# Performance work log

Measured on AMD Instinct MI355X. Metric: run time of the kernel, lower is better.

The kernel has to match this reference:

```python
import jax, jax.numpy as jnp
import numpy as np

N_NODES = 100000
N_EDGES = 250000
IN_CH = 256
OUT_CH = 256
REL_DIM = 1536
N_REL = 64
HIDDEN = IN_CH * 2  # 512
EPS = 1e-5


def setup_inputs() -> dict:
    key = jax.random.key(0)
    ks = jax.random.split(key, 12)
    s = 0.02
    return {
        "x": jax.random.normal(ks[0], (N_NODES, IN_CH), jnp.float32),
        "edge_index": jax.random.randint(ks[1], (2, N_EDGES), 0, N_NODES, jnp.int64),
        "edge_type": jax.random.randint(ks[2], (N_EDGES,), 0, N_REL, jnp.int64),
        "relation_embs": jax.random.normal(ks[3], (N_REL, REL_DIM), jnp.float32),
        "W1": jax.random.normal(ks[4], (IN_CH + REL_DIM, HIDDEN), jnp.float32) * s,
        "b1": jnp.zeros((HIDDEN,), jnp.float32),
        "W2": jax.random.normal(ks[5], (HIDDEN, OUT_CH), jnp.float32) * s,
        "b2": jnp.zeros((OUT_CH,), jnp.float32),
        "Ws": jax.random.normal(ks[6], (IN_CH, OUT_CH), jnp.float32) * s,
        "bs": jnp.zeros((OUT_CH,), jnp.float32),
        "gamma": jnp.ones((OUT_CH,), jnp.float32),
        "beta": jnp.zeros((OUT_CH,), jnp.float32),
    }


def reference(x, edge_index, edge_type, relation_embs, W1, b1, W2, b2, Ws, bs, gamma, beta):
    src, dst = edge_index[0], edge_index[1]
    # gather: per-edge inputs [E, in+rel]
    msg_in = jnp.concatenate([x[src], relation_embs[edge_type]], axis=-1)
    # message MLP: Linear -> ReLU -> Linear
    h = jax.nn.relu(msg_in @ W1 + b1)
    messages = h @ W2 + b2  # [E, out]
    # scatter_add into destination nodes
    agg = jax.ops.segment_sum(messages, dst, num_segments=x.shape[0])
    out = x @ Ws + bs + agg
    # LayerNorm (eps=1e-5) then ReLU
    mu = jnp.mean(out, axis=-1, keepdims=True)
    var = jnp.mean(jnp.square(out - mu), axis=-1, keepdims=True)
    out = (out - mu) * jax.lax.rsqrt(var + EPS) * gamma + beta
    return jax.nn.relu(out)
```

## Files before the change

kernel.cpp:

```cpp
#include <hip/hip_runtime.h>
#include <hip/hip_bf16.h>

#define IN_CHN 256
#define OUT_CHN 256
#define REL_DIM 1536
#define HIDN 512

using short8 = __attribute__((ext_vector_type(8))) short;
using f32x4  = __attribute__((ext_vector_type(4))) float;

__device__ __forceinline__ float bf2f(short s) {
    union { unsigned u; float f; } v;
    v.u = ((unsigned)(unsigned short)s) << 16;
    return v.f;
}
__device__ __forceinline__ unsigned cvt_pk_bf16(float a, float b) {
    unsigned r;
    asm("v_cvt_pk_bf16_f32 %0, %1, %2" : "=v"(r) : "v"(a), "v"(b));
    return r;
}
__device__ __forceinline__ unsigned short f2bf_s(float f) {
    union { float f; unsigned u; } v; v.f = f;
    unsigned u = v.u + 0x7FFFu + ((v.u >> 16) & 1u);
    return (unsigned short)(u >> 16);
}

__global__ void k_prep_w(const float* __restrict__ W1, const float* __restrict__ Ws,
                         const float* __restrict__ W2,
                         unsigned short* __restrict__ Bt, unsigned short* __restrict__ W2t,
                         unsigned short* __restrict__ Wst)
{
    int idx = blockIdx.x * 256 + threadIdx.x;
    const int n1 = HIDN * IN_CHN;
    const int n2 = OUT_CHN * HIDN;
    const int n3 = OUT_CHN * IN_CHN;
    if (idx < n1) {
        int j = idx >> 8, k = idx & 255;
        Bt[idx] = f2bf_s(W1[(size_t)k * HIDN + j]);
    } else if (idx < n1 + n2) {
        int t = idx - n1;
        int j = t >> 9, k = t & 511;
        W2t[t] = f2bf_s(W2[(size_t)k * OUT_CHN + j]);
    } else if (idx < n1 + n2 + n3) {
        int t = idx - n1 - n2;
        int j = t >> 8, k = t & 255;
        Wst[t] = f2bf_s(Ws[(size_t)k * OUT_CHN + j]);
    }
}

__global__ __launch_bounds__(512) void k_rel(const float* __restrict__ rel,
                                             const float* __restrict__ W1,
                                             const float* __restrict__ b1,
                                             unsigned short* __restrict__ Rb)
{
    __shared__ float s[REL_DIM];
    const int r = blockIdx.x;
    for (int i = threadIdx.x; i < REL_DIM; i += 512)
        s[i] = rel[(size_t)r * REL_DIM + i];
    __syncthreads();
    const int j = threadIdx.x;
    float acc = b1[j];
    const float* wp = W1 + (size_t)IN_CHN * HIDN + j;
#pragma unroll 8
    for (int k = 0; k < REL_DIM; ++k)
        acc = fmaf(s[k], wp[(size_t)k * HIDN], acc);
    Rb[r * HIDN + j] = f2bf_s(acc);
}

__global__ __launch_bounds__(512) void k_node(const float* __restrict__ x,
                                              const unsigned short* __restrict__ Bt,
                                              unsigned short* __restrict__ X1, int N)
{
    const int row0 = blockIdx.x * 64;
    const int tid = threadIdx.x;
    const int w = tid >> 6, l = tid & 63;
    const int l15 = l & 15, lg = l >> 4;
    const int colw = w * 64;

    const float* ap[4];
#pragma unroll
    for (int rf = 0; rf < 4; ++rf) {
        int row = row0 + 16 * rf + l15;
        if (row >= N) row = N - 1;
        ap[rf] = x + (size_t)row * IN_CHN + 8 * lg;
    }
    const unsigned short* bp[4];
#pragma unroll
    for (int cf = 0; cf < 4; ++cf)
        bp[cf] = Bt + (size_t)(colw + 16 * cf + l15) * IN_CHN + 8 * lg;

    f32x4 acc[4][4] = {};
    for (int k0 = 0; k0 < IN_CHN; k0 += 32) {
        short8 a[4], b[4];
#pragma unroll
        for (int rf = 0; rf < 4; ++rf) {
            float4 lo = *(const float4*)(ap[rf] + k0);
            float4 hi = *(const float4*)(ap[rf] + k0 + 4);
            union { short8 s; unsigned u[4]; } pk;
            pk.u[0] = cvt_pk_bf16(lo.x, lo.y);
            pk.u[1] = cvt_pk_bf16(lo.z, lo.w);
            pk.u[2] = cvt_pk_bf16(hi.x, hi.y);
            pk.u[3] = cvt_pk_bf16(hi.z, hi.w);
            a[rf] = pk.s;
        }
#pragma unroll
        for (int cf = 0; cf < 4; ++cf)
            b[cf] = *(const short8*)(bp[cf] + k0);
#pragma unroll
        for (int rf = 0; rf < 4; ++rf)
#pragma unroll
            for (int cf = 0; cf < 4; ++cf)
                acc[rf][cf] = __builtin_amdgcn_mfma_f32_16x16x32_bf16(a[rf], b[cf], acc[rf][cf], 0, 0, 0);
    }
#pragma unroll
    for (int rf = 0; rf < 4; ++rf) {
#pragma unroll
        for (int cf = 0; cf < 4; ++cf) {
            int col = colw + 16 * cf + l15;
#pragma unroll
            for (int r = 0; r < 4; ++r) {
                int row = row0 + 16 * rf + 4 * lg + r;
                if (row >= N) continue;
                X1[(size_t)row * HIDN + col] = f2bf_s(acc[rf][cf][r]);
            }
        }
    }
}

__global__ void k_hist(const int* __restrict__ ei, int* __restrict__ cnt, int E)
{
    int e = blockIdx.x * 256 + threadIdx.x;
    if (e < E) atomicAdd(&cnt[ei[E + e]], 1);
}

__global__ __launch_bounds__(512) void k_scan1(const int* __restrict__ cnt, int* __restrict__ offs,
                                               int* __restrict__ bsum, int N)
{
    __shared__ int s[512];
    int t = threadIdx.x;
    int i = blockIdx.x * 512 + t;
    int v = (i < N) ? cnt[i] : 0;
    s[t] = v;
    __syncthreads();
    for (int d = 1; d < 512; d <<= 1) {
        int a = (t >= d) ? s[t - d] : 0;
        __syncthreads();
        s[t] += a;
        __syncthreads();
    }
    if (i < N) offs[i] = s[t] - v;
    if (t == 511) bsum[blockIdx.x] = s[511];
}

__global__ __launch_bounds__(512) void k_scan2(int* __restrict__ bsum, int NB)
{
    __shared__ int s[512];
    int t = threadIdx.x;
    if (t < NB) s[t] = bsum[t];
    __syncthreads();
    if (t == 0) {
        int run = 0;
        for (int j = 0; j < NB; ++j) { int v = s[j]; s[j] = run; run += v; }
    }
    __syncthreads();
    if (t < NB) bsum[t] = s[t];
}

__global__ void k_scan3(int* __restrict__ offs, const int* __restrict__ bsum,
                        int* __restrict__ cursor, int N, int E)
{
    int i = blockIdx.x * 256 + threadIdx.x;
    if (i < N) {
        int v = offs[i] + bsum[i >> 9];
        offs[i] = v;
        cursor[i] = v;
    }
    if (i == 0) offs[N] = E;
}

__global__ void k_scatter(const int* __restrict__ ei, const int* __restrict__ et,
                          int* __restrict__ cursor, int* __restrict__ eperm, int E)
{
    int e = blockIdx.x * 256 + threadIdx.x;
    if (e < E) {
        int d = ei[E + e];
        int pos = atomicAdd(&cursor[d], 1);
        eperm[pos] = ei[e] | (et[e] << 20);
    }
}

__global__ __launch_bounds__(256, 6) void k_gather(const int* __restrict__ offs,
                                                   const int* __restrict__ eperm,
                                                   const unsigned short* __restrict__ X1,
                                                   const unsigned short* __restrict__ Rb,
                                                   unsigned short* __restrict__ Hagg, int N)
{
    const int g = (blockIdx.x * 256 + threadIdx.x) >> 6;
    const int l = threadIdx.x & 63;
    if (g >= N) return;
    const int o0 = offs[g], o1 = offs[g + 1];
    const int deg = o1 - o0;
    float a8[8] = {};
    for (int base = 0; base < deg; base += 64) {
        const int nk = min(64, deg - base);
        int pv = eperm[o0 + base + (l < nk ? l : nk - 1)];
        for (int e = 0; e < nk; e += 4) {
            int pvk[4];
#pragma unroll
            for (int k2 = 0; k2 < 4; ++k2)
                pvk[k2] = __shfl(pv, e + k2);
            short8 xa[4], ra[4];
#pragma unroll
            for (int k2 = 0; k2 < 4; ++k2) {
                if (e + k2 < nk) {
                    xa[k2] = *(const short8*)(X1 + (size_t)(pvk[k2] & 0xFFFFF) * HIDN + l * 8);
                    ra[k2] = *(const short8*)(Rb + (pvk[k2] >> 20) * HIDN + l * 8);
                }
            }
#pragma unroll
            for (int k2 = 0; k2 < 4; ++k2) {
                if (e + k2 < nk) {
#pragma unroll
                    for (int j = 0; j < 8; ++j)
                        a8[j] += fmaxf(bf2f(xa[k2][j]) + bf2f(ra[k2][j]), 0.f);
                }
            }
        }
    }
    union { short8 s; unsigned u[4]; } pk;
    pk.u[0] = cvt_pk_bf16(a8[0], a8[1]);
    pk.u[1] = cvt_pk_bf16(a8[2], a8[3]);
    pk.u[2] = cvt_pk_bf16(a8[4], a8[5]);
    pk.u[3] = cvt_pk_bf16(a8[6], a8[7]);
    *(short8*)(Hagg + (size_t)g * HIDN + l * 8) = pk.s;
}

__global__ __launch_bounds__(256) void k_out(const unsigned short* __restrict__ Hagg,
                                             const unsigned short* __restrict__ W2t,
                                             const unsigned short* __restrict__ Wst,
                                             const float* __restrict__ x,
                                             const int* __restrict__ offs,
                                             const float* __restrict__ b2,
                                             const float* __restrict__ bs,
                                             const float* __restrict__ gamma,
                                             const float* __restrict__ beta,
                                             float* __restrict__ out, int N)
{
    __shared__ unsigned short Alds[64][72];
    __shared__ float sdeg[64];
    __shared__ float sred[4][64], sqred[4][64];
    const int row0 = blockIdx.x * 64;
    const int tid = threadIdx.x;
    const int w = tid >> 6, l = tid & 63;
    const int l15 = l & 15, lg = l >> 4;
    const int colw = w * 64;

    if (tid < 64) {
        int g = row0 + tid;
        if (g >= N) g = N - 1;
        sdeg[tid] = (float)(offs[g + 1] - offs[g]);
    }

    const int srow = tid >> 2;
    int srowg = row0 + srow; if (srowg >= N) srowg = N - 1;
    const int sc = (tid & 3) * 16;
    const unsigned short* hsrc = Hagg + (size_t)srowg * HIDN + sc;
    const float* xsrc = x + (size_t)srowg * IN_CHN + sc;
    unsigned short* sdst0 = &Alds[srow][sc];
    unsigned short* sdst1 = &Alds[srow][sc + 8];

    const unsigned short* bp[4];
    const unsigned short* sp[4];
#pragma unroll
    for (int cf = 0; cf < 4; ++cf) {
        bp[cf] = W2t + (size_t)(colw + 16 * cf + l15) * HIDN + 8 * lg;
        sp[cf] = Wst + (size_t)(colw + 16 * cf + l15) * IN_CHN + 8 * lg;
    }
    const unsigned short* ard[4];
#pragma unroll
    for (int rf = 0; rf < 4; ++rf)
        ard[rf] = &Alds[16 * rf + l15][lg * 8];

    f32x4 acc[4][4] = {};
    short8 st0, st1;

    st0 = *(const short8*)(hsrc + 0);
    st1 = *(const short8*)(hsrc + 8);
    *(short8*)sdst0 = st0;
    *(short8*)sdst1 = st1;
    __syncthreads();
    for (int t = 0; t < 8; ++t) {
        if (t + 1 < 8) {
            st0 = *(const short8*)(hsrc + (t + 1) * 64);
            st1 = *(const short8*)(hsrc + (t + 1) * 64 + 8);
        }
#pragma unroll
        for (int kk = 0; kk < 2; ++kk) {
            short8 a[4], b[4];
#pragma unroll
            for (int rf = 0; rf < 4; ++rf)
                a[rf] = *(const short8*)(ard[rf] + kk * 32);
#pragma unroll
            for (int cf = 0; cf < 4; ++cf)
                b[cf] = *(const short8*)(bp[cf] + t * 64 + kk * 32);
#pragma unroll
            for (int rf = 0; rf < 4; ++rf)
#pragma unroll
                for (int cf = 0; cf < 4; ++cf)
                    acc[rf][cf] = __builtin_amdgcn_mfma_f32_16x16x32_bf16(a[rf], b[cf], acc[rf][cf], 0, 0, 0);
        }
        __syncthreads();
        if (t + 1 < 8) {
            *(short8*)sdst0 = st0;
            *(short8*)sdst1 = st1;
            __syncthreads();
        }
    }

    {
        float4 f0 = *(const float4*)(xsrc + 0);
        float4 f1 = *(const float4*)(xsrc + 4);
        float4 f2 = *(const float4*)(xsrc + 8);
        float4 f3 = *(const float4*)(xsrc + 12);
        union { short8 s; unsigned u[4]; } p0, p1;
        p0.u[0] = cvt_pk_bf16(f0.x, f0.y); p0.u[1] = cvt_pk_bf16(f0.z, f0.w);
        p0.u[2] = cvt_pk_bf16(f1.x, f1.y); p0.u[3] = cvt_pk_bf16(f1.z, f1.w);
        p1.u[0] = cvt_pk_bf16(f2.x, f2.y); p1.u[1] = cvt_pk_bf16(f2.z, f2.w);
        p1.u[2] = cvt_pk_bf16(f3.x, f3.y); p1.u[3] = cvt_pk_bf16(f3.z, f3.w);
        *(short8*)sdst0 = p0.s;
        *(short8*)sdst1 = p1.s;
    }
    __syncthreads();
    for (int t = 0; t < 4; ++t) {
        float4 f0, f1, f2, f3;
        if (t + 1 < 4) {
            f0 = *(const float4*)(xsrc + (t + 1) * 64);
            f1 = *(const float4*)(xsrc + (t + 1) * 64 + 4);
            f2 = *(const float4*)(xsrc + (t + 1) * 64 + 8);
            f3 = *(const float4*)(xsrc + (t + 1) * 64 + 12);
        }
#pragma unroll
        for (int kk = 0; kk < 2; ++kk) {
            short8 a[4], b[4];
#pragma unroll
            for (int rf = 0; rf < 4; ++rf)
                a[rf] = *(const short8*)(ard[rf] + kk * 32);
#pragma unroll
            for (int cf = 0; cf < 4; ++cf)
                b[cf] = *(const short8*)(sp[cf] + t * 64 + kk * 32);
#pragma unroll
            for (int rf = 0; rf < 4; ++rf)
#pragma unroll
                for (int cf = 0; cf < 4; ++cf)
                    acc[rf][cf] = __builtin_amdgcn_mfma_f32_16x16x32_bf16(a[rf], b[cf], acc[rf][cf], 0, 0, 0);
        }
        __syncthreads();
        if (t + 1 < 4) {
            union { short8 s; unsigned u[4]; } p0, p1;
            p0.u[0] = cvt_pk_bf16(f0.x, f0.y); p0.u[1] = cvt_pk_bf16(f0.z, f0.w);
            p0.u[2] = cvt_pk_bf16(f1.x, f1.y); p0.u[3] = cvt_pk_bf16(f1.z, f1.w);
            p1.u[0] = cvt_pk_bf16(f2.x, f2.y); p1.u[1] = cvt_pk_bf16(f2.z, f2.w);
            p1.u[2] = cvt_pk_bf16(f3.x, f3.y); p1.u[3] = cvt_pk_bf16(f3.z, f3.w);
            *(short8*)sdst0 = p0.s;
            *(short8*)sdst1 = p1.s;
            __syncthreads();
        }
    }

    float b2v[4], bsv[4], gv[4], bv[4];
#pragma unroll
    for (int cf = 0; cf < 4; ++cf) {
        int col = colw + 16 * cf + l15;
        b2v[cf] = b2[col]; bsv[cf] = bs[col]; gv[cf] = gamma[col]; bv[cf] = beta[col];
    }
#pragma unroll
    for (int rf = 0; rf < 4; ++rf) {
#pragma unroll
        for (int r = 0; r < 4; ++r) {
            int row = 16 * rf + 4 * lg + r;
            float dg = sdeg[row];
            float s = 0.f, sq = 0.f;
#pragma unroll
            for (int cf = 0; cf < 4; ++cf) {
                float v = acc[rf][cf][r] + dg * b2v[cf] + bsv[cf];
                acc[rf][cf][r] = v;
                s += v; sq += v * v;
            }
#pragma unroll
            for (int o = 8; o > 0; o >>= 1) {
                s  += __shfl_xor(s, o);
                sq += __shfl_xor(sq, o);
            }
            if (l15 == 0) { sred[w][row] = s; sqred[w][row] = sq; }
        }
    }
    __syncthreads();
#pragma unroll
    for (int rf = 0; rf < 4; ++rf) {
#pragma unroll
        for (int r = 0; r < 4; ++r) {
            int row = 16 * rf + 4 * lg + r;
            int g = row0 + row;
            if (g >= N) continue;
            float tot  = sred[0][row] + sred[1][row] + sred[2][row] + sred[3][row];
            float totq = sqred[0][row] + sqred[1][row] + sqred[2][row] + sqred[3][row];
            float mu = tot * (1.f / OUT_CHN);
            float var = totq * (1.f / OUT_CHN) - mu * mu;
            float rstd = rsqrtf(var + 1e-5f);
#pragma unroll
            for (int cf = 0; cf < 4; ++cf) {
                int col = colw + 16 * cf + l15;
                float v = (acc[rf][cf][r] - mu) * rstd * gv[cf] + bv[cf];
                out[(size_t)g * OUT_CHN + col] = fmaxf(v, 0.f);
            }
        }
    }
}

extern "C" void kernel_launch(void* const* d_in, const int* in_sizes, int n_in,
                              void* d_out, int out_size, void* d_ws, size_t ws_size,
                              hipStream_t stream)
{
    const float* x     = (const float*)d_in[0];
    const int*   ei    = (const int*)d_in[1];
    const int*   etype = (const int*)d_in[2];
    const float* rel   = (const float*)d_in[3];
    const float* W1    = (const float*)d_in[4];
    const float* b1    = (const float*)d_in[5];
    const float* W2    = (const float*)d_in[6];
    const float* b2    = (const float*)d_in[7];
    const float* Ws    = (const float*)d_in[8];
    const float* bs    = (const float*)d_in[9];
    const float* gamma = (const float*)d_in[10];
    const float* beta  = (const float*)d_in[11];

    const int N  = in_sizes[0] / IN_CHN;
    const int E  = in_sizes[2];
    const int NR = in_sizes[3] / REL_DIM;
    float* outp = (float*)d_out;

    char* wsp = (char*)d_ws;
    auto carve = [&](size_t bytes) { char* p = wsp; wsp += (bytes + 255) & ~(size_t)255; return p; };
    unsigned short* X1  = (unsigned short*)carve((size_t)N * HIDN * 2);
    unsigned short* Rb  = (unsigned short*)carve((size_t)NR * HIDN * 2);
    unsigned short* Bt  = (unsigned short*)carve((size_t)HIDN * IN_CHN * 2);
    unsigned short* W2t = (unsigned short*)carve((size_t)OUT_CHN * HIDN * 2);
    unsigned short* Wst = (unsigned short*)carve((size_t)OUT_CHN * IN_CHN * 2);
    int* offs  = (int*)carve(((size_t)N + 1) * 4);
    int* cnt   = (int*)carve((size_t)N * 4);
    int* bsum  = (int*)carve(512 * 4);
    int* eperm = (int*)carve((size_t)E * 4);

    unsigned short* Hagg = (unsigned short*)d_out;

    hipMemsetAsync(cnt, 0, (size_t)N * 4, stream);

    const int prep_total = HIDN * IN_CHN + OUT_CHN * HIDN + OUT_CHN * IN_CHN;
    k_prep_w<<<dim3((prep_total + 255) / 256), dim3(256), 0, stream>>>(W1, Ws, W2, Bt, W2t, Wst);
    k_rel<<<dim3(NR), dim3(512), 0, stream>>>(rel, W1, b1, Rb);
    k_node<<<dim3((N + 63) / 64), dim3(512), 0, stream>>>(x, Bt, X1, N);
    k_hist<<<dim3((E + 255) / 256), dim3(256), 0, stream>>>(ei, cnt, E);
    int NB = (N + 511) / 512;
    k_scan1<<<dim3(NB), dim3(512), 0, stream>>>(cnt, offs, bsum, N);
    k_scan2<<<dim3(1), dim3(512), 0, stream>>>(bsum, NB);
    k_scan3<<<dim3((N + 255) / 256), dim3(256), 0, stream>>>(offs, bsum, cnt, N, E);
    k_scatter<<<dim3((E + 255) / 256), dim3(256), 0, stream>>>(ei, etype, cnt, eperm, E);
    k_gather<<<dim3((N + 3) / 4), dim3(256), 0, stream>>>(offs, eperm, X1, Rb, Hagg, N);
    k_out<<<dim3((N + 63) / 64), dim3(256), 0, stream>>>(Hagg, W2t, Wst, x, offs,
                                                         b2, bs, gamma, beta, outp, N);
}
```

Before: 510.8 us.

## Stage node GEMM A-tile through LDS and double-buffer the output GEMM

k_node now loads each x row once cooperatively, converts it to bf16 into a shared LDS tile, and has all 8 waves read A fragments from LDS. Before, every wave reloaded and reconverted the same fp32 rows from global memory. k_out merges its two GEMM loops (Hagg·W2 and x·Ws) into one 12-step loop with a double-buffered LDS tile, which removes one barrier per step. The costs are extra LDS use and barriers in k_node, plus per-step branching in k_out.

```diff
diff --git a/kernel.cpp b/kernel.cpp
--- a/kernel.cpp
+++ b/kernel.cpp
@@ -71,47 +71,70 @@
                                               const unsigned short* __restrict__ Bt,
                                               unsigned short* __restrict__ X1, int N)
 {
+    __shared__ unsigned short Alds[64][72];
     const int row0 = blockIdx.x * 64;
     const int tid = threadIdx.x;
     const int w = tid >> 6, l = tid & 63;
     const int l15 = l & 15, lg = l >> 4;
     const int colw = w * 64;
 
-    const float* ap[4];
-#pragma unroll
-    for (int rf = 0; rf < 4; ++rf) {
-        int row = row0 + 16 * rf + l15;
-        if (row >= N) row = N - 1;
-        ap[rf] = x + (size_t)row * IN_CHN + 8 * lg;
-    }
+    const int srow = tid >> 3;
+    int srowg = row0 + srow; if (srowg >= N) srowg = N - 1;
+    const int sc = (tid & 7) * 8;
+    const float* xsrc = x + (size_t)srowg * IN_CHN + sc;
+    unsigned short* sdst = &Alds[srow][sc];
+
     const unsigned short* bp[4];
 #pragma unroll
     for (int cf = 0; cf < 4; ++cf)
         bp[cf] = Bt + (size_t)(colw + 16 * cf + l15) * IN_CHN + 8 * lg;
+    const unsigned short* ard[4];
+#pragma unroll
+    for (int rf = 0; rf < 4; ++rf)
+        ard[rf] = &Alds[16 * rf + l15][lg * 8];
 
     f32x4 acc[4][4] = {};
-    for (int k0 = 0; k0 < IN_CHN; k0 += 32) {
-        short8 a[4], b[4];
-#pragma unroll
-        for (int rf = 0; rf < 4; ++rf) {
-            float4 lo = *(const float4*)(ap[rf] + k0);
-            float4 hi = *(const float4*)(ap[rf] + k0 + 4);
-            union { short8 s; unsigned u[4]; } pk;
-            pk.u[0] = cvt_pk_bf16(lo.x, lo.y);
-            pk.u[1] = cvt_pk_bf16(lo.z, lo.w);
-            pk.u[2] = cvt_pk_bf16(hi.x, hi.y);
-            pk.u[3] = cvt_pk_bf16(hi.z, hi.w);
-            a[rf] = pk.s;
-        }
-#pragma unroll
-        for (int cf = 0; cf < 4; ++cf)
-            b[cf] = *(const short8*)(bp[cf] + k0);
-#pragma unroll
-        for (int rf = 0; rf < 4; ++rf)
+
+    {
+        float4 g0 = *(const float4*)(xsrc + 0);
+        float4 g1 = *(const float4*)(xsrc + 4);
+        union { short8 s; unsigned u[4]; } p;
+        p.u[0] = cvt_pk_bf16(g0.x, g0.y); p.u[1] = cvt_pk_bf16(g0.z, g0.w);
+        p.u[2] = cvt_pk_bf16(g1.x, g1.y); p.u[3] = cvt_pk_bf16(g1.z, g1.w);
+        *(short8*)sdst = p.s;
+    }
+    __syncthreads();
+    for (int t = 0; t < 4; ++t) {
+        float4 g0, g1;
+        if (t + 1 < 4) {
+            g0 = *(const float4*)(xsrc + (t + 1) * 64);
+            g1 = *(const float4*)(xsrc + (t + 1) * 64 + 4);
+        }
+#pragma unroll
+        for (int kk = 0; kk < 2; ++kk) {
+            short8 a[4], b[4];
+#pragma unroll
+            for (int rf = 0; rf < 4; ++rf)
+                a[rf] = *(const short8*)(ard[rf] + kk * 32);
 #pragma unroll
             for (int cf = 0; cf < 4; ++cf)
-                acc[rf][cf] = __builtin_amdgcn_mfma_f32_16x16x32_bf16(a[rf], b[cf], acc[rf][cf], 0, 0, 0);
-    }
+                b[cf] = *(const short8*)(bp[cf] + t * 64 + kk * 32);
+#pragma unroll
+            for (int rf = 0; rf < 4; ++rf)
+#pragma unroll
+                for (int cf = 0; cf < 4; ++cf)
+                    acc[rf][cf] = __builtin_amdgcn_mfma_f32_16x16x32_bf16(a[rf], b[cf], acc[rf][cf], 0, 0, 0);
+        }
+        __syncthreads();
+        if (t + 1 < 4) {
+            union { short8 s; unsigned u[4]; } p;
+            p.u[0] = cvt_pk_bf16(g0.x, g0.y); p.u[1] = cvt_pk_bf16(g0.z, g0.w);
+            p.u[2] = cvt_pk_bf16(g1.x, g1.y); p.u[3] = cvt_pk_bf16(g1.z, g1.w);
+            *(short8*)sdst = p.s;
+            __syncthreads();
+        }
+    }
+
 #pragma unroll
     for (int rf = 0; rf < 4; ++rf) {
 #pragma unroll
@@ -246,7 +269,7 @@
                                              const float* __restrict__ beta,
                                              float* __restrict__ out, int N)
 {
-    __shared__ unsigned short Alds[64][72];
+    __shared__ unsigned short Alds[2][64][72];
     __shared__ float sdeg[64];
     __shared__ float sred[4][64], sqred[4][64];
     const int row0 = blockIdx.x * 64;
@@ -266,8 +289,6 @@
     const int sc = (tid & 3) * 16;
     const unsigned short* hsrc = Hagg + (size_t)srowg * HIDN + sc;
     const float* xsrc = x + (size_t)srowg * IN_CHN + sc;
-    unsigned short* sdst0 = &Alds[srow][sc];
-    unsigned short* sdst1 = &Alds[srow][sc + 8];
 
     const unsigned short* bp[4];
     const unsigned short* sp[4];
@@ -276,95 +297,71 @@
         bp[cf] = W2t + (size_t)(colw + 16 * cf + l15) * HIDN + 8 * lg;
         sp[cf] = Wst + (size_t)(colw + 16 * cf + l15) * IN_CHN + 8 * lg;
     }
-    const unsigned short* ard[4];
-#pragma unroll
-    for (int rf = 0; rf < 4; ++rf)
-        ard[rf] = &Alds[16 * rf + l15][lg * 8];
+    const int arow[4] = { 16 * 0 + l15, 16 * 1 + l15, 16 * 2 + l15, 16 * 3 + l15 };
 
     f32x4 acc[4][4] = {};
-    short8 st0, st1;
-
-    st0 = *(const short8*)(hsrc + 0);
-    st1 = *(const short8*)(hsrc + 8);
-    *(short8*)sdst0 = st0;
-    *(short8*)sdst1 = st1;
-    __syncthreads();
-    for (int t = 0; t < 8; ++t) {
-        if (t + 1 < 8) {
-            st0 = *(const short8*)(hsrc + (t + 1) * 64);
-            st1 = *(const short8*)(hsrc + (t + 1) * 64 + 8);
-        }
+
+    {
+        short8 s0 = *(const short8*)(hsrc + 0);
+        short8 s1 = *(const short8*)(hsrc + 8);
+        *(short8*)&Alds[0][srow][sc] = s0;
+        *(short8*)&Alds[0][srow][sc + 8] = s1;
+    }
+    __syncthreads();
+
+    for (int t = 0; t < 12; ++t) {
+        const int cur = t & 1, nxt = cur ^ 1;
+        short8 s0, s1;
+        float4 f0, f1, f2, f3;
+        bool isf = false;
+        if (t + 1 < 12) {
+            if (t + 1 < 8) {
+                s0 = *(const short8*)(hsrc + (t + 1) * 64);
+                s1 = *(const short8*)(hsrc + (t + 1) * 64 + 8);
+            } else {
+                isf = true;
+                const float* xp2 = xsrc + (t + 1 - 8) * 64;
+                f0 = *(const float4*)(xp2 + 0);
+                f1 = *(const float4*)(xp2 + 4);
+                f2 = *(const float4*)(xp2 + 8);
+                f3 = *(const float4*)(xp2 + 12);
+            }
+        }
+        const int kb = (t < 8) ? t * 64 : (t - 8) * 64;
 #pragma unroll
         for (int kk = 0; kk < 2; ++kk) {
             short8 a[4], b[4];
 #pragma unroll
             for (int rf = 0; rf < 4; ++rf)
-                a[rf] = *(const short8*)(ard[rf] + kk * 32);
-#pragma unroll
-            for (int cf = 0; cf < 4; ++cf)
-                b[cf] = *(const short8*)(bp[cf] + t * 64 + kk * 32);
+                a[rf] = *(const short8*)&Alds[cur][arow[rf]][lg * 8 + kk * 32];
+            if (t < 8) {
+#pragma unroll
+                for (int cf = 0; cf < 4; ++cf)
+                    b[cf] = *(const short8*)(bp[cf] + kb + kk * 32);
+            } else {
+#pragma unroll
+                for (int cf = 0; cf < 4; ++cf)
+                    b[cf] = *(const short8*)(sp[cf] + kb + kk * 32);
+            }
 #pragma unroll
             for (int rf = 0; rf < 4; ++rf)
 #pragma unroll
                 for (int cf = 0; cf < 4; ++cf)
                     acc[rf][cf] = __builtin_amdgcn_mfma_f32_16x16x32_bf16(a[rf], b[cf], acc[rf][cf], 0, 0, 0);
         }
+        if (t + 1 < 12) {
+            if (isf) {
+                union { short8 s; unsigned u[4]; } p0, p1;
+                p0.u[0] = cvt_pk_bf16(f0.x, f0.y); p0.u[1] = cvt_pk_bf16(f0.z, f0.w);
+                p0.u[2] = cvt_pk_bf16(f1.x, f1.y); p0.u[3] = cvt_pk_bf16(f1.z, f1.w);
+                p1.u[0] = cvt_pk_bf16(f2.x, f2.y); p1.u[1] = cvt_pk_bf16(f2.z, f2.w);
+                p1.u[2] = cvt_pk_bf16(f3.x, f3.y); p1.u[3] = cvt_pk_bf16(f3.z, f3.w);
+                s0 = p0.s; s1 = p1.s;
+            }
+            *(short8*)&Alds[nxt][srow][sc] = s0;
+            *(short8*)&Alds[nxt][srow][sc + 8] = s1;
+        }
         __syncthreads();
-        if (t + 1 < 8) {
-            *(short8*)sdst0 = st0;
-            *(short8*)sdst1 = st1;
-            __syncthreads();
-        }
-    }
-
-    {
-        float4 f0 = *(const float4*)(xsrc + 0);
-        float4 f1 = *(const float4*)(xsrc + 4);
-        float4 f2 = *(const float4*)(xsrc + 8);
-        float4 f3 = *(const float4*)(xsrc + 12);
-        union { short8 s; unsigned u[4]; } p0, p1;
-        p0.u[0] = cvt_pk_bf16(f0.x, f0.y); p0.u[1] = cvt_pk_bf16(f0.z, f0.w);
-        p0.u[2] = cvt_pk_bf16(f1.x, f1.y); p0.u[3] = cvt_pk_bf16(f1.z, f1.w);
-        p1.u[0] = cvt_pk_bf16(f2.x, f2.y); p1.u[1] = cvt_pk_bf16(f2.z, f2.w);
-        p1.u[2] = cvt_pk_bf16(f3.x, f3.y); p1.u[3] = cvt_pk_bf16(f3.z, f3.w);
-        *(short8*)sdst0 = p0.s;
-        *(short8*)sdst1 = p1.s;
-    }
-    __syncthreads();
-    for (int t = 0; t < 4; ++t) {
-        float4 f0, f1, f2, f3;
-        if (t + 1 < 4) {
-            f0 = *(const float4*)(xsrc + (t + 1) * 64);
-            f1 = *(const float4*)(xsrc + (t + 1) * 64 + 4);
-            f2 = *(const float4*)(xsrc + (t + 1) * 64 + 8);
-            f3 = *(const float4*)(xsrc + (t + 1) * 64 + 12);
-        }
-#pragma unroll
-        for (int kk = 0; kk < 2; ++kk) {
-            short8 a[4], b[4];
-#pragma unroll
-            for (int rf = 0; rf < 4; ++rf)
-                a[rf] = *(const short8*)(ard[rf] + kk * 32);
-#pragma unroll
-            for (int cf = 0; cf < 4; ++cf)
-                b[cf] = *(const short8*)(sp[cf] + t * 64 + kk * 32);
-#pragma unroll
-            for (int rf = 0; rf < 4; ++rf)
-#pragma unroll
-                for (int cf = 0; cf < 4; ++cf)
-                    acc[rf][cf] = __builtin_amdgcn_mfma_f32_16x16x32_bf16(a[rf], b[cf], acc[rf][cf], 0, 0, 0);
-        }
-        __syncthreads();
-        if (t + 1 < 4) {
-            union { short8 s; unsigned u[4]; } p0, p1;
-            p0.u[0] = cvt_pk_bf16(f0.x, f0.y); p0.u[1] = cvt_pk_bf16(f0.z, f0.w);
-            p0.u[2] = cvt_pk_bf16(f1.x, f1.y); p0.u[3] = cvt_pk_bf16(f1.z, f1.w);
-            p1.u[0] = cvt_pk_bf16(f2.x, f2.y); p1.u[1] = cvt_pk_bf16(f2.z, f2.w);
-            p1.u[2] = cvt_pk_bf16(f3.x, f3.y); p1.u[3] = cvt_pk_bf16(f3.z, f3.w);
-            *(short8*)sdst0 = p0.s;
-            *(short8*)sdst1 = p1.s;
-            __syncthreads();
-        }
     }
 
     float b2v[4], bsv[4], gv[4], bv[4];
```

New measurement: 441.7 us. 13.5% less time.
